# Optimization experiments

Hardware: AMD Instinct MI355X
Metric: run time of the kernel (lower is better)

Reference implementation:

```python
import jax, jax.numpy as jnp
import numpy as np

N_NODES = 50000


def _sage_conv(x, edge_index, Wl, bl, Wr):
    # PyG SAGEConv with mean aggregation:
    #   out_i = Wl @ mean_{j in N(i)} x_j + bl + Wr @ x_i
    src, dst = edge_index[0], edge_index[1]
    msgs = x[src]                                            # [E, d] gather
    summed = jax.ops.segment_sum(msgs, dst, num_segments=N_NODES)   # [N, d]
    count = jax.ops.segment_sum(jnp.ones((edge_index.shape[1],), x.dtype),
                                dst, num_segments=N_NODES)          # [N]
    agg = summed / jnp.maximum(count, 1.0)[:, None]          # mean, 0 for isolated nodes
    return agg @ Wl.T + bl + x @ Wr.T


def setup_inputs() -> dict:
    key = jax.random.key(0)
    k1, k2, k3, k4, k5 = jax.random.split(key, 5)
    d = 128
    E = 640000
    x = jax.random.normal(k1, (N_NODES, d), dtype=jnp.float32)
    edge_index = jax.random.randint(k2, (2, E), 0, N_NODES, dtype=jnp.int64)
    s = 1.0 / np.sqrt(d)
    Wl = jax.random.uniform(k3, (d, d), jnp.float32, -s, s)
    bl = jax.random.uniform(k4, (d,), jnp.float32, -s, s)
    Wr = jax.random.uniform(k5, (d, d), jnp.float32, -s, s)
    return {"x": x, "edge_index": edge_index, "Wl": Wl, "bl": bl, "Wr": Wr}


def reference(x, edge_index, Wl, bl, Wr):
    # forward in the source applies conv1 twice (conv2 is unused)
    h = _sage_conv(x, edge_index, Wl, bl, Wr)
    h = jax.nn.relu(h)
    h = _sage_conv(h, edge_index, Wl, bl, Wr)
    return h
```

## Files before the change

### kernel.cpp

```cpp
#include <hip/hip_runtime.h>

#define NN 50000
#define D 128
#define CAP 48

typedef short bf16x8 __attribute__((ext_vector_type(8)));
typedef float f32x16 __attribute__((ext_vector_type(16)));

__device__ __forceinline__ unsigned bf16r(float f) {
    unsigned u = __float_as_uint(f);
    return (u + 0x7FFFu + ((u >> 16) & 1u)) >> 16;
}
__device__ __forceinline__ float bflo(unsigned u) { return __uint_as_float(u << 16); }
__device__ __forceinline__ float bfhi(unsigned u) { return __uint_as_float(u & 0xFFFF0000u); }


__global__ void zero_k(uint4* __restrict__ p, int nq) {
    int i = blockIdx.x * 256 + threadIdx.x;
    if (i < nq) { uint4 z = {0, 0, 0, 0}; p[i] = z; }
}


__global__ void fillfix_k(const int* __restrict__ ei, int E,
                          int* __restrict__ count, int* __restrict__ csrf) {
    int e = blockIdx.x * 256 + threadIdx.x;
    if (e < E) {
        int d = ei[E + e];
        int slot = atomicAdd(&count[d], 1);
        csrf[d * CAP + slot] = ei[e];
    }
}


__global__ void wtbcvt_k(const float* __restrict__ Wl, const float* __restrict__ Wr,
                         uint* __restrict__ wb,
                         const float* __restrict__ x, uint* __restrict__ xb, int nquad) {
    if (blockIdx.x < 64) {
        int i = blockIdx.x * 256 + threadIdx.x;
        int nrow = i >> 7;
        int k = (i & 127) * 2;
        const float* W = (k < 128) ? Wl : Wr;
        int kk = k & 127;
        uint lo = bf16r(W[nrow * 128 + kk]);
        uint hi = bf16r(W[nrow * 128 + kk + 1]);
        wb[i] = (hi << 16) | lo;
    } else {
        int i = (blockIdx.x - 64) * 256 + threadIdx.x;
        if (i >= nquad) return;
        float4 v = ((const float4*)x)[i];
        uint2 p;
        p.x = (bf16r(v.y) << 16) | bf16r(v.x);
        p.y = (bf16r(v.w) << 16) | bf16r(v.z);
        ((uint2*)xb)[i] = p;
    }
}


#define ACC8(v)                                                         \
    s0 += bflo(v.x); s1 += bfhi(v.x); s2 += bflo(v.y); s3 += bfhi(v.y); \
    s4 += bflo(v.z); s5 += bfhi(v.z); s6 += bflo(v.w); s7 += bfhi(v.w);

__global__ __launch_bounds__(256) void fused_layer_k(
    const uint4* __restrict__ in4,
    const int* __restrict__ count,
    const int* __restrict__ csrf,
    const ushort* __restrict__ Wb,
    const float* __restrict__ bl,
    float* __restrict__ out,
    ushort* __restrict__ hb,
    int N, int relu) {
    __shared__ uint4 At[32][16];

    int tid = threadIdx.x;
    int mt  = blockIdx.x;

    int lnode = tid >> 4;
    int c16   = tid & 15;
    #pragma unroll
    for (int g = 0; g < 2; ++g) {
        int lrow = g * 16 + lnode;
        int n = mt * 32 + lrow;
        float s0=0,s1=0,s2=0,s3=0,s4=0,s5=0,s6=0,s7=0;
        float inv = 0.f;
        if (n < N) {
            int deg = count[n];
            int ro  = n * CAP;
            int i = 0;
            for (; i + 4 <= deg; i += 4) {
                int e0 = csrf[ro+i+0], e1 = csrf[ro+i+1];
                int e2 = csrf[ro+i+2], e3 = csrf[ro+i+3];
                uint4 v0 = in4[(size_t)e0 * 16 + c16];
                uint4 v1 = in4[(size_t)e1 * 16 + c16];
                uint4 v2 = in4[(size_t)e2 * 16 + c16];
                uint4 v3 = in4[(size_t)e3 * 16 + c16];
                ACC8(v0); ACC8(v1); ACC8(v2); ACC8(v3);
            }
            for (; i + 2 <= deg; i += 2) {
                int e0 = csrf[ro + i], e1 = csrf[ro + i + 1];
                uint4 v0 = in4[(size_t)e0 * 16 + c16];
                uint4 v1 = in4[(size_t)e1 * 16 + c16];
                ACC8(v0); ACC8(v1);
            }
            if (i < deg) {
                uint4 v0 = in4[(size_t)csrf[ro + i] * 16 + c16];
                ACC8(v0);
            }
            inv = (deg > 0) ? (1.f / (float)deg) : 0.f;
        }
        uint4 r;
        r.x = (bf16r(s1 * inv) << 16) | bf16r(s0 * inv);
        r.y = (bf16r(s3 * inv) << 16) | bf16r(s2 * inv);
        r.z = (bf16r(s5 * inv) << 16) | bf16r(s4 * inv);
        r.w = (bf16r(s7 * inv) << 16) | bf16r(s6 * inv);
        At[lrow][c16 ^ (lrow & 7)] = r;
    }
    __syncthreads();

    int wid   = tid >> 6;
    int lane  = tid & 63;
    int col   = lane & 31;
    int khalf = lane >> 5;
    int nfeat = wid * 32 + col;

    bf16x8 B[16], A[16];
    const ushort* wrow = Wb + (size_t)nfeat * 256 + khalf * 8;
    #pragma unroll
    for (int ks = 0; ks < 16; ++ks)
        B[ks] = *reinterpret_cast<const bf16x8*>(wrow + ks * 16);

    #pragma unroll
    for (int ks = 0; ks < 8; ++ks) {
        int cc = (ks * 2 + khalf) ^ (col & 7);
        A[ks] = *reinterpret_cast<const bf16x8*>(&At[col][cc]);
    }
    int rowc = min(mt * 32 + col, N - 1);
    const ushort* ar1 = (const ushort*)in4 + (size_t)rowc * 128 + khalf * 8;
    #pragma unroll
    for (int ks = 0; ks < 8; ++ks)
        A[8 + ks] = *reinterpret_cast<const bf16x8*>(ar1 + ks * 16);

    f32x16 acc = {};
    #pragma unroll
    for (int ks = 0; ks < 16; ++ks)
        acc = __builtin_amdgcn_mfma_f32_32x32x16_bf16(A[ks], B[ks], acc, 0, 0, 0);

    float bias = bl[nfeat];
    #pragma unroll
    for (int r2 = 0; r2 < 16; ++r2) {
        int rr = (r2 & 3) + 8 * (r2 >> 2) + 4 * khalf;
        int gm = mt * 32 + rr;
        if (gm < N) {
            float v = acc[r2] + bias;
            if (relu) v = fmaxf(v, 0.f);
            if (out) __builtin_nontemporal_store(v, out + (size_t)gm * 128 + nfeat);
            if (hb)  hb[(size_t)gm * 128 + nfeat] = (ushort)bf16r(v);
        }
    }
}

extern "C" void kernel_launch(void* const* d_in, const int* in_sizes, int n_in,
                              void* d_out, int out_size, void* d_ws, size_t ws_size,
                              hipStream_t stream) {
    const float* x  = (const float*)d_in[0];
    const int*   ei = (const int*)d_in[1];
    const float* Wl = (const float*)d_in[2];
    const float* bl = (const float*)d_in[3];
    const float* Wr = (const float*)d_in[4];
    float* out = (float*)d_out;

    const int N = NN;
    const int E = in_sizes[1] / 2;
    const int NPAD = 50016;

    int* ws    = (int*)d_ws;
    int* count = ws;
    int* csrf  = ws + N;
    uint* wb   = (uint*)(ws + N + N * CAP);
    uint* xb   = wb + 128 * 128;
    uint* hb   = xb + (size_t)NPAD * 64;

    int eb = (E + 255) / 256;

    zero_k<<<(N / 4 + 255) / 256, 256, 0, stream>>>((uint4*)count, N / 4);
    fillfix_k<<<eb, 256, 0, stream>>>(ei, E, count, csrf);
    wtbcvt_k<<<64 + (N * 32 + 255) / 256, 256, 0, stream>>>(Wl, Wr, wb, x, xb, N * 32);

    int mtiles = (N + 31) / 32;
    fused_layer_k<<<mtiles, 256, 0, stream>>>((const uint4*)xb, count, csrf,
                                              (const ushort*)wb, bl,
                                              (float*)nullptr, (ushort*)hb, N, 1);
    fused_layer_k<<<mtiles, 256, 0, stream>>>((const uint4*)hb, count, csrf,
                                              (const ushort*)wb, bl,
                                              out, (ushort*)nullptr, N, 0);
}
```

Before: 155.3 us.

## Build compact CSR via two-level shared-memory counting sort instead of global atomics

Replaces the fixed-capacity padded adjacency build, which used one global atomicAdd per edge, with a two-level counting sort. Edges are first bucketed by dst>>8 using per-block shared histograms and a single-block scan, then sorted within each bucket in shared memory to produce a rowptr array and a 16-bit source index array. The aim is to cut global atomic contention and halve the index bytes the gather kernels read. The zero kernel is folded into the histogram/convert kernel, but the pipeline gains a serial single-block scan and another launch, and 16-bit indices only work because N is below 65536.

```diff
diff --git a/kernel.cpp b/kernel.cpp
--- a/kernel.cpp
+++ b/kernel.cpp
@@ -2,7 +2,7 @@
 
 #define NN 50000
 #define D 128
-#define CAP 48
+#define BLK_E 4096
 
 typedef short bf16x8 __attribute__((ext_vector_type(8)));
 typedef float f32x16 __attribute__((ext_vector_type(16)));
@@ -15,28 +15,35 @@
 __device__ __forceinline__ float bfhi(unsigned u) { return __uint_as_float(u & 0xFFFF0000u); }
 
 
-__global__ void zero_k(uint4* __restrict__ p, int nq) {
-    int i = blockIdx.x * 256 + threadIdx.x;
-    if (i < nq) { uint4 z = {0, 0, 0, 0}; p[i] = z; }
-}
-
-
-__global__ void fillfix_k(const int* __restrict__ ei, int E,
-                          int* __restrict__ count, int* __restrict__ csrf) {
-    int e = blockIdx.x * 256 + threadIdx.x;
-    if (e < E) {
-        int d = ei[E + e];
-        int slot = atomicAdd(&count[d], 1);
-        csrf[d * CAP + slot] = ei[e];
-    }
-}
-
-
-__global__ void wtbcvt_k(const float* __restrict__ Wl, const float* __restrict__ Wr,
-                         uint* __restrict__ wb,
-                         const float* __restrict__ x, uint* __restrict__ xb, int nquad) {
-    if (blockIdx.x < 64) {
-        int i = blockIdx.x * 256 + threadIdx.x;
+__global__ void passA_k(const int* __restrict__ ei, int E,
+                        int* __restrict__ counts, int nebl,
+                        const float* __restrict__ Wl, const float* __restrict__ Wr,
+                        uint* __restrict__ wb,
+                        const float* __restrict__ x, uint* __restrict__ xb, int nquad) {
+    int bid = blockIdx.x;
+    int t = threadIdx.x;
+    if (bid < nebl) {
+        __shared__ int dh[256];
+        dh[t] = 0;
+        __syncthreads();
+        const int* dst = ei + E;
+        int base = bid * BLK_E + t * 16;
+        if (base + 16 <= E) {
+            #pragma unroll
+            for (int q = 0; q < 4; ++q) {
+                int4 d4 = *(const int4*)(dst + base + q * 4);
+                atomicAdd(&dh[d4.x >> 8], 1);
+                atomicAdd(&dh[d4.y >> 8], 1);
+                atomicAdd(&dh[d4.z >> 8], 1);
+                atomicAdd(&dh[d4.w >> 8], 1);
+            }
+        } else {
+            for (int e = base; e < E; ++e) atomicAdd(&dh[dst[e] >> 8], 1);
+        }
+        __syncthreads();
+        counts[bid * 256 + t] = dh[t];
+    } else if (bid < nebl + 64) {
+        int i = (bid - nebl) * 256 + t;
         int nrow = i >> 7;
         int k = (i & 127) * 2;
         const float* W = (k < 128) ? Wl : Wr;
@@ -45,7 +52,7 @@
         uint hi = bf16r(W[nrow * 128 + kk + 1]);
         wb[i] = (hi << 16) | lo;
     } else {
-        int i = (blockIdx.x - 64) * 256 + threadIdx.x;
+        int i = (bid - nebl - 64) * 256 + t;
         if (i >= nquad) return;
         float4 v = ((const float4*)x)[i];
         uint2 p;
@@ -56,14 +63,113 @@
 }
 
 
+__global__ void passB_k(int* __restrict__ counts, int nebl,
+                        int* __restrict__ binBase) {
+    __shared__ int sm[256];
+    int t = threadIdx.x;
+    int run = 0;
+    for (int b = 0; b < nebl; b += 8) {
+        int v[8];
+        #pragma unroll
+        for (int j = 0; j < 8; ++j)
+            v[j] = (b + j < nebl) ? counts[(b + j) * 256 + t] : 0;
+        #pragma unroll
+        for (int j = 0; j < 8; ++j) {
+            if (b + j < nebl) counts[(b + j) * 256 + t] = run;
+            run += v[j];
+        }
+    }
+    int v = run;
+    sm[t] = v;
+    __syncthreads();
+    for (int off = 1; off < 256; off <<= 1) {
+        int a = (t >= off) ? sm[t - off] : 0;
+        __syncthreads();
+        sm[t] += a;
+        __syncthreads();
+    }
+    binBase[t] = sm[t] - v;
+    if (t == 255) binBase[256] = sm[255];
+}
+
+
+__global__ void passC_k(const int* __restrict__ ei, int E,
+                        const int* __restrict__ counts,
+                        const int* __restrict__ binBase,
+                        uint* __restrict__ upack, int nebl) {
+    __shared__ int cur[256];
+    int t = threadIdx.x, bid = blockIdx.x;
+    cur[t] = counts[bid * 256 + t] + binBase[t];
+    __syncthreads();
+    const int* dst = ei + E;
+    const int* src = ei;
+    int base = bid * BLK_E + t * 16;
+    if (base + 16 <= E) {
+        #pragma unroll
+        for (int q = 0; q < 4; ++q) {
+            int4 d4 = *(const int4*)(dst + base + q * 4);
+            int4 s4 = *(const int4*)(src + base + q * 4);
+            int p;
+            p = atomicAdd(&cur[d4.x >> 8], 1);
+            upack[p] = ((uint)(d4.x & 255) << 16) | (uint)s4.x;
+            p = atomicAdd(&cur[d4.y >> 8], 1);
+            upack[p] = ((uint)(d4.y & 255) << 16) | (uint)s4.y;
+            p = atomicAdd(&cur[d4.z >> 8], 1);
+            upack[p] = ((uint)(d4.z & 255) << 16) | (uint)s4.z;
+            p = atomicAdd(&cur[d4.w >> 8], 1);
+            upack[p] = ((uint)(d4.w & 255) << 16) | (uint)s4.w;
+        }
+    } else {
+        for (int e = base; e < E; ++e) {
+            int d = dst[e];
+            int p = atomicAdd(&cur[d >> 8], 1);
+            upack[p] = ((uint)(d & 255) << 16) | (uint)src[e];
+        }
+    }
+}
+
+
+__global__ void passD_k(const uint* __restrict__ upack,
+                        const int* __restrict__ binBase,
+                        int* __restrict__ rowptr, ushort* __restrict__ csrW, int N) {
+    __shared__ int lh[256], sm[256], cur[256];
+    int p = blockIdx.x, t = threadIdx.x;
+    int s0 = binBase[p], s1 = binBase[p + 1];
+    lh[t] = 0;
+    __syncthreads();
+    for (int e = s0 + t; e < s1; e += 256)
+        atomicAdd(&lh[upack[e] >> 16], 1);
+    __syncthreads();
+    int v = lh[t];
+    sm[t] = v;
+    __syncthreads();
+    for (int off = 1; off < 256; off <<= 1) {
+        int a = (t >= off) ? sm[t - off] : 0;
+        __syncthreads();
+        sm[t] += a;
+        __syncthreads();
+    }
+    int lbase = sm[t] - v;
+    int d = p * 256 + t;
+    if (d <= N) rowptr[d] = s0 + lbase;
+    cur[t] = lbase;
+    __syncthreads();
+    for (int e = s0 + t; e < s1; e += 256) {
+        uint u = upack[e];
+        int r = atomicAdd(&cur[u >> 16], 1);
+        csrW[s0 + r] = (ushort)(u & 0xFFFFu);
+    }
+}
+
+
 #define ACC8(v)                                                         \
     s0 += bflo(v.x); s1 += bfhi(v.x); s2 += bflo(v.y); s3 += bfhi(v.y); \
     s4 += bflo(v.z); s5 += bfhi(v.z); s6 += bflo(v.w); s7 += bfhi(v.w);
 
 __global__ __launch_bounds__(256) void fused_layer_k(
     const uint4* __restrict__ in4,
-    const int* __restrict__ count,
-    const int* __restrict__ csrf,
+    const int* __restrict__ rowptr,
+    const ushort* __restrict__ csrW,
     const ushort* __restrict__ Wb,
     const float* __restrict__ bl,
     float* __restrict__ out,
@@ -83,12 +189,12 @@
         float s0=0,s1=0,s2=0,s3=0,s4=0,s5=0,s6=0,s7=0;
         float inv = 0.f;
         if (n < N) {
-            int deg = count[n];
-            int ro  = n * CAP;
+            int ro  = rowptr[n];
+            int deg = rowptr[n + 1] - ro;
             int i = 0;
             for (; i + 4 <= deg; i += 4) {
-                int e0 = csrf[ro+i+0], e1 = csrf[ro+i+1];
-                int e2 = csrf[ro+i+2], e3 = csrf[ro+i+3];
+                int e0 = csrW[ro+i+0], e1 = csrW[ro+i+1];
+                int e2 = csrW[ro+i+2], e3 = csrW[ro+i+3];
                 uint4 v0 = in4[(size_t)e0 * 16 + c16];
                 uint4 v1 = in4[(size_t)e1 * 16 + c16];
                 uint4 v2 = in4[(size_t)e2 * 16 + c16];
@@ -96,13 +202,13 @@
                 ACC8(v0); ACC8(v1); ACC8(v2); ACC8(v3);
             }
             for (; i + 2 <= deg; i += 2) {
-                int e0 = csrf[ro + i], e1 = csrf[ro + i + 1];
+                int e0 = csrW[ro + i], e1 = csrW[ro + i + 1];
                 uint4 v0 = in4[(size_t)e0 * 16 + c16];
                 uint4 v1 = in4[(size_t)e1 * 16 + c16];
                 ACC8(v0); ACC8(v1);
             }
             if (i < deg) {
-                uint4 v0 = in4[(size_t)csrf[ro + i] * 16 + c16];
+                uint4 v0 = in4[(size_t)csrW[ro + i] * 16 + c16];
                 ACC8(v0);
             }
             inv = (deg > 0) ? (1.f / (float)deg) : 0.f;
@@ -172,24 +278,32 @@
     const int E = in_sizes[1] / 2;
     const int NPAD = 50016;
 
-    int* ws    = (int*)d_ws;
-    int* count = ws;
-    int* csrf  = ws + N;
-    uint* wb   = (uint*)(ws + N + N * CAP);
-    uint* xb   = wb + 128 * 128;
-    uint* hb   = xb + (size_t)NPAD * 64;
-
-    int eb = (E + 255) / 256;
-
-    zero_k<<<(N / 4 + 255) / 256, 256, 0, stream>>>((uint4*)count, N / 4);
-    fillfix_k<<<eb, 256, 0, stream>>>(ei, E, count, csrf);
-    wtbcvt_k<<<64 + (N * 32 + 255) / 256, 256, 0, stream>>>(Wl, Wr, wb, x, xb, N * 32);
+    int nebl = (E + BLK_E - 1) / BLK_E;
+
+    int*    ws      = (int*)d_ws;
+    int*    rowptr  = ws;
+    int*    counts  = ws + 50016;
+    int*    binBase = counts + nebl * 256;
+    uint*   upack   = (uint*)(binBase + 260);
+    ushort* csrW    = (ushort*)(upack + E);
+    uint*   wb      = (uint*)(csrW + E);
+    uint*   xb      = wb + 128 * 128;
+    uint*   hb      = xb + (size_t)NPAD * 64;
+
+    int nquad = N * 32;
+    int cvtb  = (nquad + 255) / 256;
+
+    passA_k<<<nebl + 64 + cvtb, 256, 0, stream>>>(ei, E, counts, nebl,
+                                                  Wl, Wr, wb, x, xb, nquad);
+    passB_k<<<1, 256, 0, stream>>>(counts, nebl, binBase);
+    passC_k<<<nebl, 256, 0, stream>>>(ei, E, counts, binBase, upack, nebl);
+    passD_k<<<(N + 256) / 256, 256, 0, stream>>>(upack, binBase, rowptr, csrW, N);
 
     int mtiles = (N + 31) / 32;
-    fused_layer_k<<<mtiles, 256, 0, stream>>>((const uint4*)xb, count, csrf,
+    fused_layer_k<<<mtiles, 256, 0, stream>>>((const uint4*)xb, rowptr, csrW,
                                               (const ushort*)wb, bl,
                                               (float*)nullptr, (ushort*)hb, N, 1);
-    fused_layer_k<<<mtiles, 256, 0, stream>>>((const uint4*)hb, count, csrf,
+    fused_layer_k<<<mtiles, 256, 0, stream>>>((const uint4*)hb, rowptr, csrW,
                                               (const ushort*)wb, bl,
                                               out, (ushort*)nullptr, N, 0);
 }
```

New measurement: 139.4 us, median of 2. -10.3%, faster.
